# Performance work log

Measured on AMD Instinct MI355X. Metric: run time of the kernel, lower is better.

The kernel has to match this reference:

```python
import jax, jax.numpy as jnp
import numpy as np

N, D, IN, HID, OUT = 50000, 16, 128, 128, 64

def setup_inputs() -> dict:
    key = jax.random.key(0)
    ks = jax.random.split(key, 16)
    s = 0.05
    return {
        'feats':   jax.random.normal(ks[0], (N, IN), jnp.float32),
        'nbr':     jax.random.randint(ks[1], (N, D), 0, N, jnp.int32),
        'w_ih1':   jax.random.normal(ks[2], (4*IN, IN), jnp.float32)*s,
        'w_hh1':   jax.random.normal(ks[3], (4*IN, IN), jnp.float32)*s,
        'b_ih1':   jax.random.normal(ks[4], (4*IN,), jnp.float32)*s,
        'b_hh1':   jax.random.normal(ks[5], (4*IN,), jnp.float32)*s,
        'w_self1': jax.random.normal(ks[6], (HID, IN), jnp.float32)*s,
        'w_neigh1':jax.random.normal(ks[7], (HID, IN), jnp.float32)*s,
        'b1':      jax.random.normal(ks[8], (HID,), jnp.float32)*s,
        'w_ih2':   jax.random.normal(ks[9], (4*HID, HID), jnp.float32)*s,
        'w_hh2':   jax.random.normal(ks[10], (4*HID, HID), jnp.float32)*s,
        'b_ih2':   jax.random.normal(ks[11], (4*HID,), jnp.float32)*s,
        'b_hh2':   jax.random.normal(ks[12], (4*HID,), jnp.float32)*s,
        'w_self2': jax.random.normal(ks[13], (OUT, HID), jnp.float32)*s,
        'w_neigh2':jax.random.normal(ks[14], (OUT, HID), jnp.float32)*s,
        'b2':      jax.random.normal(ks[15], (OUT,), jnp.float32)*s,
    }

def _lstm_agg(m, w_ih, w_hh, b_ih, b_hh):
    # m: [N, D, F] gathered neighbor features; LSTM hidden size == F (DGL lstm reducer).
    n, d, f = m.shape
    b = b_ih + b_hh
    def step(carry, x_t):
        h, c = carry
        gates = x_t @ w_ih.T + h @ w_hh.T + b  # [N, 4F]
        i, fg, g, o = jnp.split(gates, 4, axis=-1)  # PyTorch gate order i,f,g,o
        i = jax.nn.sigmoid(i); fg = jax.nn.sigmoid(fg)
        g = jnp.tanh(g); o = jax.nn.sigmoid(o)
        c = fg * c + i * g
        h = o * jnp.tanh(c)
        return (h, c), None
    z = jnp.zeros((n, f), m.dtype)
    (h, _), _ = jax.lax.scan(step, (z, z), jnp.swapaxes(m, 0, 1))  # scan over degree axis
    return h  # [N, F] final hidden state

def _sage_conv(x, nbr, w_ih, w_hh, b_ih, b_hh, w_self, w_neigh, bias):
    m = x[nbr]  # [N, D, F] gather neighbor features
    h_neigh = _lstm_agg(m, w_ih, w_hh, b_ih, b_hh)
    return x @ w_self.T + h_neigh @ w_neigh.T + bias

def reference(feats, nbr, w_ih1, w_hh1, b_ih1, b_hh1, w_self1, w_neigh1, b1,
              w_ih2, w_hh2, b_ih2, b_hh2, w_self2, w_neigh2, b2):
    h = _sage_conv(feats, nbr, w_ih1, w_hh1, b_ih1, b_hh1, w_self1, w_neigh1, b1)
    h = jax.nn.relu(h)
    h = _sage_conv(h, nbr, w_ih2, w_hh2, b_ih2, b_hh2, w_self2, w_neigh2, b2)
    return jax.nn.sigmoid(h)
```

## Files before the change

### kernel.cpp

```cpp
#include <hip/hip_runtime.h>
#include <cstdint>
#include <cstddef>


constexpr int IN  = 128;
constexpr int DEG = 16;
#define LOG2E       1.4426950408889634f
#define TWO_LOG2E   2.8853900817779268f
#define NEG2_LOG2E -2.8853900817779268f

typedef short bf16x8 __attribute__((ext_vector_type(8)));
typedef float f32x4  __attribute__((ext_vector_type(4)));
typedef float f32x16 __attribute__((ext_vector_type(16)));
typedef unsigned int u32x4 __attribute__((ext_vector_type(4)));
typedef unsigned int u32x2 __attribute__((ext_vector_type(2)));

__device__ __forceinline__ float fsigmoid(float x) {
    float e = __expf(-x);
    return __builtin_amdgcn_rcpf(1.0f + e);
}
__device__ __forceinline__ uint32_t pack2bf16(float a, float b) {
    uint32_t ua = __float_as_uint(a) + 0x8000u;
    uint32_t ub = __float_as_uint(b) + 0x8000u;
    return (ua >> 16) | (ub & 0xFFFF0000u);
}


__global__ void k_pack_all(const float* __restrict__ w0, u32x4* __restrict__ f0,
                           const float* __restrict__ w1, u32x4* __restrict__ f1,
                           const float* __restrict__ w2, u32x4* __restrict__ f2,
                           const float* __restrict__ w3, u32x4* __restrict__ f3) {
    int gt = blockIdx.x * 256 + threadIdx.x;
    int which = gt >> 13;
    int tid  = gt & 8191;
    const float* wsrc = (which == 0) ? w0 : (which == 1) ? w1 : (which == 2) ? w2 : w3;
    u32x4* frag = (which == 0) ? f0 : (which == 1) ? f1 : (which == 2) ? f2 : f3;
    int lane = tid & 63;
    float v[8];
    int row;
    if ((which & 1) == 0) {
        int tile = (tid >> 6) & 15;
        int kst  = tid >> 10;
        row = tile * 32 + (lane & 31);
        int kbase = kst * 16 + (lane >> 5) * 8;
#pragma unroll
        for (int j = 0; j < 8; ++j) v[j] = wsrc[row * 128 + kbase + j];
    } else {
        int f  = tid >> 6;
        int ks = f & 3;
        int w8 = (f >> 2) & 7;
        int g  = f >> 5;
        row = g * 128 + w8 * 16 + (lane & 15);
        int kbase = ks * 32 + (lane >> 4) * 8;
#pragma unroll
        for (int j = 0; j < 8; ++j) v[j] = wsrc[row * 128 + kbase + j];
    }
    const float sc = ((row >> 7) == 2) ? TWO_LOG2E : LOG2E;
#pragma unroll
    for (int j = 0; j < 8; ++j) v[j] *= sc;
    u32x4 d;
    d.x = pack2bf16(v[0], v[1]);
    d.y = pack2bf16(v[2], v[3]);
    d.z = pack2bf16(v[4], v[5]);
    d.w = pack2bf16(v[6], v[7]);
    frag[tid] = d;
}

__global__ void k_pack_out(const float* __restrict__ ws1, const float* __restrict__ wn1,
                           u32x4* __restrict__ f1,
                           const float* __restrict__ ws2, const float* __restrict__ wn2,
                           u32x4* __restrict__ f2) {
    int t = blockIdx.x * 256 + threadIdx.x;
    int lane = t & 63;
    int row  = lane & 15;
    int kb   = (lane >> 4) * 8;
    float v[8];
    const float* ws; const float* wn; u32x4* dst; int p;
    if (t < 4096) { ws = ws1; wn = wn1; dst = f1; p = t; }
    else          { ws = ws2; wn = wn2; dst = f2; p = t - 4096; }
    int ks  = (p >> 6) & 7;
    int och = (p >> 9) * 16 + row;
    int kbase = ks * 32 + kb;
#pragma unroll
    for (int j = 0; j < 8; ++j) {
        int k = kbase + j;
        v[j] = (k < 128) ? ws[och * 128 + k] : wn[och * 128 + k - 128];
    }
    u32x4 d;
    d.x = pack2bf16(v[0], v[1]);
    d.y = pack2bf16(v[2], v[3]);
    d.z = pack2bf16(v[4], v[5]);
    d.w = pack2bf16(v[6], v[7]);
    dst[p] = d;
}

template <int CVT>
__global__ __launch_bounds__(256, 2) void k_xu(
    const void*   __restrict__ xin,
    ushort*       __restrict__ xbf,
    const u32x4*  __restrict__ wih,
    const float*  __restrict__ b_ih,
    const float*  __restrict__ b_hh,
    u32x2*        __restrict__ xu,
    int N)
{
    __shared__ u32x4 a_buf[16][66];

    const int tid   = threadIdx.x;
    const int lane  = tid & 63;
    const int w     = tid >> 6;
    const int mrow  = lane & 31;
    const int khalf = lane >> 5;
    const int node0 = blockIdx.x * 64;

    u32x4 wreg[8][4];
#pragma unroll
    for (int kst = 0; kst < 8; ++kst)
#pragma unroll
        for (int g = 0; g < 4; ++g)
            wreg[kst][g] = wih[(kst * 16 + g * 4 + w) * 64 + lane];

    float binit[4];
#pragma unroll
    for (int g = 0; g < 4; ++g) {
        int jj = g * 128 + w * 32 + mrow;
        binit[g] = (b_ih[jj] + b_hh[jj]) * ((g == 2) ? TWO_LOG2E : LOG2E);
    }

    {
        int m_st = tid >> 2, c4 = tid & 3;
        int gn = node0 + m_st; if (gn >= N) gn = N - 1;
        if constexpr (CVT) {
            const float* src = (const float*)xin + (size_t)gn * IN;
#pragma unroll
            for (int q = 0; q < 4; ++q) {
                int kg = q * 4 + c4;
                float4 f0 = *(const float4*)(src + kg * 8);
                float4 f1 = *(const float4*)(src + kg * 8 + 4);
                u32x4 d;
                d.x = pack2bf16(f0.x, f0.y);
                d.y = pack2bf16(f0.z, f0.w);
                d.z = pack2bf16(f1.x, f1.y);
                d.w = pack2bf16(f1.z, f1.w);
                a_buf[kg][m_st] = d;
                *(u32x4*)(xbf + (size_t)gn * IN + kg * 8) = d;
            }
        } else {
            const u32x4* src = (const u32x4*)((const ushort*)xin + (size_t)gn * IN);
#pragma unroll
            for (int q = 0; q < 4; ++q) {
                int kg = q * 4 + c4;
                a_buf[kg][m_st] = src[kg];
            }
        }
    }
    __syncthreads();

    const int coff = w * 32 + mrow;
#pragma unroll 1
    for (int Mt = 0; Mt < 2; ++Mt) {
        f32x16 acc[4];
#pragma unroll
        for (int g = 0; g < 4; ++g)
#pragma unroll
            for (int r = 0; r < 16; ++r) acc[g][r] = binit[g];

#pragma unroll
        for (int kst = 0; kst < 8; ++kst) {
            bf16x8 a = __builtin_bit_cast(bf16x8, a_buf[kst * 2 + khalf][Mt * 32 + mrow]);
#pragma unroll
            for (int g = 0; g < 4; ++g)
                acc[g] = __builtin_amdgcn_mfma_f32_32x32x16_bf16(
                    a, __builtin_bit_cast(bf16x8, wreg[kst][g]), acc[g], 0, 0, 0);
        }

#pragma unroll
        for (int r = 0; r < 16; ++r) {
            int m = Mt * 32 + (r & 3) + 8 * (r >> 2) + 4 * khalf;
            u32x2 d;
            d.x = pack2bf16(acc[0][r], acc[1][r]);
            d.y = pack2bf16(acc[2][r], acc[3][r]);
            xu[(size_t)(node0 + m) * 128 + coff] = d;
        }
    }
}

template <int NOUT, int ACT, typename OutT>
__global__ __launch_bounds__(512, 4) void k_lstm_fused(
    const u32x2*  __restrict__ xu,
    const int*    __restrict__ nbr,
    const u32x4*  __restrict__ whh,
    const u32x4*  __restrict__ wout,
    const float*  __restrict__ bout,
    const ushort* __restrict__ x_in,
    OutT*         __restrict__ out,
    int N)
{
    constexpr int HSTR = 272;
    __shared__ alignas(16) char h_lds[2][16 * HSTR];
    __shared__ uint32_t idxs[DEG * 16];

    const int tid  = threadIdx.x;
    const int lane = tid & 63;
    const int w    = tid >> 6;
    const int col  = lane & 15;
    const int l4   = lane >> 4;
    const int node0 = blockIdx.x * 16;

    if (tid < DEG * 16) {
        int m = tid & 15, t = tid >> 4;
        int gn = node0 + m; if (gn >= N) gn = N - 1;
        idxs[t * 16 + m] = (uint32_t)nbr[gn * DEG + t] << 10;
    }
    if (tid < 16 * HSTR / 16)
        ((u32x4*)h_lds[0])[tid] = u32x4{0u, 0u, 0u, 0u};

    u32x4 wreg[4][4];
#pragma unroll
    for (int g = 0; g < 4; ++g)
#pragma unroll
        for (int ks = 0; ks < 4; ++ks)
            wreg[g][ks] = whh[((g * 8 + w) * 4 + ks) * 64 + lane];

    float cst[4];
#pragma unroll
    for (int r = 0; r < 4; ++r) cst[r] = 0.0f;

    const char* xu_c = (const char*)xu;
    const uint32_t goff = (uint32_t)(w * 128 + l4 * 32);
    const int rd0 = col * HSTR + l4 * 16;
    const int wr0 = col * HSTR + w * 32 + l4 * 8;

    __syncthreads();

    u32x4 vv[2];
    {
        const char* p0 = xu_c + idxs[col] + goff;
        vv[0] = *(const u32x4*)(p0);
        vv[1] = *(const u32x4*)(p0 + 16);
    }

#pragma unroll 1
    for (int t = 0; t < DEG; ++t) {
        const char* hr = h_lds[t & 1];
        char*       hw = h_lds[(t + 1) & 1];

        f32x4 acc[4];
#pragma unroll
        for (int q = 0; q < 4; ++q) {
            uint32_t px = vv[q >> 1][(q & 1) * 2];
            uint32_t py = vv[q >> 1][(q & 1) * 2 + 1];
            acc[0][q] = __uint_as_float(px << 16);
            acc[1][q] = __uint_as_float(px & 0xFFFF0000u);
            acc[2][q] = __uint_as_float(py << 16);
            acc[3][q] = __uint_as_float(py & 0xFFFF0000u);
        }

        if (t + 1 < DEG) {
            const char* p0 = xu_c + idxs[(t + 1) * 16 + col] + goff;
            vv[0] = *(const u32x4*)(p0);
            vv[1] = *(const u32x4*)(p0 + 16);
        }

#pragma unroll
        for (int ks = 0; ks < 4; ++ks) {
            bf16x8 b = *(const bf16x8*)(hr + rd0 + ks * 64);
#pragma unroll
            for (int g = 0; g < 4; ++g)
                acc[g] = __builtin_amdgcn_mfma_f32_16x16x32_bf16(
                    __builtin_bit_cast(bf16x8, wreg[g][ks]), b, acc[g], 0, 0, 0);
        }

        float hv[4];
#pragma unroll
        for (int q = 0; q < 4; ++q) {
            float Ei = __builtin_amdgcn_exp2f(-acc[0][q]);
            float Eg = __builtin_amdgcn_exp2f(-acc[2][q]);
            float Ef = __builtin_amdgcn_exp2f(-acc[1][q]);
            float p  = (1.0f + Ei) * (1.0f + Eg);
            float num = __fmaf_rn(cst[q], p, (1.0f - Eg) * (1.0f + Ef));
            float cv = num * __builtin_amdgcn_rcpf(p * (1.0f + Ef));
            cst[q] = cv;
            float Eo = __builtin_amdgcn_exp2f(-acc[3][q]);
            float Ec = __builtin_amdgcn_exp2f(cv * NEG2_LOG2E);
            hv[q] = (1.0f - Ec) *
                    __builtin_amdgcn_rcpf((1.0f + Eo) * (1.0f + Ec));
        }
        u32x2 hp;
        hp.x = pack2bf16(hv[0], hv[1]);
        hp.y = pack2bf16(hv[2], hv[3]);
        *(u32x2*)(hw + wr0) = hp;

        __syncthreads();
    }

    if (NOUT == 128 || w < 4) {
        const char* hf = h_lds[0];
        const int otile = (NOUT == 128) ? w : (w & 3);
        const int och0  = otile * 16 + l4 * 4;
        const float4 bq = *(const float4*)(bout + och0);
        const int gn = node0 + col;
        const int gx = (gn < N) ? gn : (N - 1);
        f32x4 acc = {bq.x, bq.y, bq.z, bq.w};
#pragma unroll
        for (int ks = 0; ks < 8; ++ks) {
            u32x4 af = wout[(otile * 8 + ks) * 64 + lane];
            bf16x8 bf_;
            if (ks < 4)
                bf_ = *(const bf16x8*)((const char*)x_in + (size_t)gx * 256 +
                                       ks * 64 + l4 * 16);
            else
                bf_ = *(const bf16x8*)(hf + col * HSTR + (ks - 4) * 64 + l4 * 16);
            acc = __builtin_amdgcn_mfma_f32_16x16x32_bf16(
                __builtin_bit_cast(bf16x8, af), bf_, acc, 0, 0, 0);
        }
        if (gn < N) {
            float av[4];
#pragma unroll
            for (int q = 0; q < 4; ++q)
                av[q] = (ACT == 0) ? fmaxf(acc[q], 0.0f) : fsigmoid(acc[q]);
            if constexpr (sizeof(OutT) == 2) {
                u32x2 o;
                o.x = pack2bf16(av[0], av[1]);
                o.y = pack2bf16(av[2], av[3]);
                *(u32x2*)((ushort*)out + (size_t)gn * NOUT + och0) = o;
            } else {
                f32x4 o = {av[0], av[1], av[2], av[3]};
                *(f32x4*)((float*)out + (size_t)gn * NOUT + och0) = o;
            }
        }
    }
}

extern "C" void kernel_launch(void* const* d_in, const int* in_sizes, int n_in,
                              void* d_out, int out_size, void* d_ws, size_t ws_size,
                              hipStream_t stream)
{
    const float* feats    = (const float*)d_in[0];
    const int*   nbr      = (const int*)  d_in[1];
    const float* w_ih1    = (const float*)d_in[2];
    const float* w_hh1    = (const float*)d_in[3];
    const float* b_ih1    = (const float*)d_in[4];
    const float* b_hh1    = (const float*)d_in[5];
    const float* w_self1  = (const float*)d_in[6];
    const float* w_neigh1 = (const float*)d_in[7];
    const float* b1       = (const float*)d_in[8];
    const float* w_ih2    = (const float*)d_in[9];
    const float* w_hh2    = (const float*)d_in[10];
    const float* b_ih2    = (const float*)d_in[11];
    const float* b_hh2    = (const float*)d_in[12];
    const float* w_self2  = (const float*)d_in[13];
    const float* w_neigh2 = (const float*)d_in[14];
    const float* b2       = (const float*)d_in[15];
    float* out = (float*)d_out;

    const int N = in_sizes[0] / IN;
    const long long Nceil = (N + 63) & ~63LL;

    char* ws = (char*)d_ws;
    size_t off = 0;
    auto alloc = [&](size_t bytes) -> void* {
        void* p = (void*)(ws + off);
        off += (bytes + 255) & ~(size_t)255;
        return p;
    };
    u32x4*  wfrag_ih1 = (u32x4*)alloc(8192 * 16);
    u32x4*  wfrag_hh1 = (u32x4*)alloc(8192 * 16);
    u32x4*  wfrag_ih2 = (u32x4*)alloc(8192 * 16);
    u32x4*  wfrag_hh2 = (u32x4*)alloc(8192 * 16);
    u32x4*  wofrag1   = (u32x4*)alloc(4096 * 16);
    u32x4*  wofrag2   = (u32x4*)alloc(2048 * 16);
    ushort* feats_bf  = (ushort*)alloc((size_t)N * 128 * 2);
    ushort* out1      = (ushort*)alloc((size_t)N * 128 * 2);
    u32x2*  xu_buf    = (u32x2*)alloc((size_t)Nceil * 128 * 8);

    k_pack_all<<<dim3(128), dim3(256), 0, stream>>>(w_ih1, wfrag_ih1, w_hh1, wfrag_hh1,
                                                    w_ih2, wfrag_ih2, w_hh2, wfrag_hh2);
    k_pack_out<<<dim3(24), dim3(256), 0, stream>>>(w_self1, w_neigh1, wofrag1,
                                                   w_self2, w_neigh2, wofrag2);

    const int nblk64 = (int)(Nceil / 64);
    const int nblk16 = (N + 15) / 16;

    k_xu<1><<<dim3(nblk64), dim3(256), 0, stream>>>(feats, feats_bf, wfrag_ih1, b_ih1, b_hh1, xu_buf, N);
    k_lstm_fused<128, 0, ushort><<<dim3(nblk16), dim3(512), 0, stream>>>(
        xu_buf, nbr, wfrag_hh1, wofrag1, b1, feats_bf, out1, N);

    k_xu<0><<<dim3(nblk64), dim3(256), 0, stream>>>(out1, nullptr, wfrag_ih2, b_ih2, b_hh2, xu_buf, N);
    k_lstm_fused<64, 1, float><<<dim3(nblk16), dim3(512), 0, stream>>>(
        xu_buf, nbr, wfrag_hh2, wofrag2, b2, out1, out, N);
}
```

Baseline: 473.5 us.

## Make LSTM fused kernels persistent with atomic tile scheduling

Both fused LSTM kernels now launch a fixed grid of 512 blocks. Each block repeatedly claims 16-node tiles through a global atomic counter, which `k_pack_all` zeroes. This amortizes loading the recurrent weight fragments into registers across many tiles and removes block launch overhead. In exchange it adds an atomic plus an extra barrier per tile and caps residency at about two blocks per CU, which may reduce latency hiding in the barrier-heavy recurrence.

```diff
diff --git a/kernel.cpp b/kernel.cpp
--- a/kernel.cpp
+++ b/kernel.cpp
@@ -29,8 +29,10 @@
 __global__ void k_pack_all(const float* __restrict__ w0, u32x4* __restrict__ f0,
                            const float* __restrict__ w1, u32x4* __restrict__ f1,
                            const float* __restrict__ w2, u32x4* __restrict__ f2,
-                           const float* __restrict__ w3, u32x4* __restrict__ f3) {
+                           const float* __restrict__ w3, u32x4* __restrict__ f3,
+                           uint32_t* __restrict__ counters) {
     int gt = blockIdx.x * 256 + threadIdx.x;
+    if (gt < 2) counters[gt] = 0u;
     int which = gt >> 13;
     int tid  = gt & 8191;
     const float* wsrc = (which == 0) ? w0 : (which == 1) ? w1 : (which == 2) ? w2 : w3;
@@ -194,26 +196,19 @@
     const float*  __restrict__ bout,
     const ushort* __restrict__ x_in,
     OutT*         __restrict__ out,
-    int N)
+    uint32_t*     __restrict__ counter,
+    int ntiles, int N)
 {
     constexpr int HSTR = 272;
     __shared__ alignas(16) char h_lds[2][16 * HSTR];
     __shared__ uint32_t idxs[DEG * 16];
+    __shared__ int tile_s;
 
     const int tid  = threadIdx.x;
     const int lane = tid & 63;
     const int w    = tid >> 6;
     const int col  = lane & 15;
     const int l4   = lane >> 4;
-    const int node0 = blockIdx.x * 16;
-
-    if (tid < DEG * 16) {
-        int m = tid & 15, t = tid >> 4;
-        int gn = node0 + m; if (gn >= N) gn = N - 1;
-        idxs[t * 16 + m] = (uint32_t)nbr[gn * DEG + t] << 10;
-    }
-    if (tid < 16 * HSTR / 16)
-        ((u32x4*)h_lds[0])[tid] = u32x4{0u, 0u, 0u, 0u};
 
     u32x4 wreg[4][4];
 #pragma unroll
@@ -221,112 +216,128 @@
 #pragma unroll
         for (int ks = 0; ks < 4; ++ks)
             wreg[g][ks] = whh[((g * 8 + w) * 4 + ks) * 64 + lane];
-
-    float cst[4];
-#pragma unroll
-    for (int r = 0; r < 4; ++r) cst[r] = 0.0f;
 
     const char* xu_c = (const char*)xu;
     const uint32_t goff = (uint32_t)(w * 128 + l4 * 32);
     const int rd0 = col * HSTR + l4 * 16;
     const int wr0 = col * HSTR + w * 32 + l4 * 8;
 
-    __syncthreads();
-
-    u32x4 vv[2];
-    {
-        const char* p0 = xu_c + idxs[col] + goff;
-        vv[0] = *(const u32x4*)(p0);
-        vv[1] = *(const u32x4*)(p0 + 16);
-    }
-
-#pragma unroll 1
-    for (int t = 0; t < DEG; ++t) {
-        const char* hr = h_lds[t & 1];
-        char*       hw = h_lds[(t + 1) & 1];
-
-        f32x4 acc[4];
-#pragma unroll
-        for (int q = 0; q < 4; ++q) {
-            uint32_t px = vv[q >> 1][(q & 1) * 2];
-            uint32_t py = vv[q >> 1][(q & 1) * 2 + 1];
-            acc[0][q] = __uint_as_float(px << 16);
-            acc[1][q] = __uint_as_float(px & 0xFFFF0000u);
-            acc[2][q] = __uint_as_float(py << 16);
-            acc[3][q] = __uint_as_float(py & 0xFFFF0000u);
-        }
-
-        if (t + 1 < DEG) {
-            const char* p0 = xu_c + idxs[(t + 1) * 16 + col] + goff;
+    for (;;) {
+        if (tid == 0) tile_s = (int)atomicAdd(counter, 1u);
+        __syncthreads();
+        const int tile = tile_s;
+        if (tile >= ntiles) break;
+        const int node0 = tile * 16;
+
+        if (tid < DEG * 16) {
+            int m = tid & 15, t = tid >> 4;
+            int gn = node0 + m; if (gn >= N) gn = N - 1;
+            idxs[t * 16 + m] = (uint32_t)nbr[gn * DEG + t] << 10;
+        }
+        if (tid < 16 * HSTR / 16)
+            ((u32x4*)h_lds[0])[tid] = u32x4{0u, 0u, 0u, 0u};
+
+        float cst[4];
+#pragma unroll
+        for (int r = 0; r < 4; ++r) cst[r] = 0.0f;
+
+        __syncthreads();
+
+        u32x4 vv[2];
+        {
+            const char* p0 = xu_c + idxs[col] + goff;
             vv[0] = *(const u32x4*)(p0);
             vv[1] = *(const u32x4*)(p0 + 16);
         }
 
-#pragma unroll
-        for (int ks = 0; ks < 4; ++ks) {
-            bf16x8 b = *(const bf16x8*)(hr + rd0 + ks * 64);
-#pragma unroll
-            for (int g = 0; g < 4; ++g)
-                acc[g] = __builtin_amdgcn_mfma_f32_16x16x32_bf16(
-                    __builtin_bit_cast(bf16x8, wreg[g][ks]), b, acc[g], 0, 0, 0);
-        }
-
-        float hv[4];
-#pragma unroll
-        for (int q = 0; q < 4; ++q) {
-            float Ei = __builtin_amdgcn_exp2f(-acc[0][q]);
-            float Eg = __builtin_amdgcn_exp2f(-acc[2][q]);
-            float Ef = __builtin_amdgcn_exp2f(-acc[1][q]);
-            float p  = (1.0f + Ei) * (1.0f + Eg);
-            float num = __fmaf_rn(cst[q], p, (1.0f - Eg) * (1.0f + Ef));
-            float cv = num * __builtin_amdgcn_rcpf(p * (1.0f + Ef));
-            cst[q] = cv;
-            float Eo = __builtin_amdgcn_exp2f(-acc[3][q]);
-            float Ec = __builtin_amdgcn_exp2f(cv * NEG2_LOG2E);
-            hv[q] = (1.0f - Ec) *
-                    __builtin_amdgcn_rcpf((1.0f + Eo) * (1.0f + Ec));
-        }
-        u32x2 hp;
-        hp.x = pack2bf16(hv[0], hv[1]);
-        hp.y = pack2bf16(hv[2], hv[3]);
-        *(u32x2*)(hw + wr0) = hp;
-
-        __syncthreads();
-    }
-
-    if (NOUT == 128 || w < 4) {
-        const char* hf = h_lds[0];
-        const int otile = (NOUT == 128) ? w : (w & 3);
-        const int och0  = otile * 16 + l4 * 4;
-        const float4 bq = *(const float4*)(bout + och0);
-        const int gn = node0 + col;
-        const int gx = (gn < N) ? gn : (N - 1);
-        f32x4 acc = {bq.x, bq.y, bq.z, bq.w};
-#pragma unroll
-        for (int ks = 0; ks < 8; ++ks) {
-            u32x4 af = wout[(otile * 8 + ks) * 64 + lane];
-            bf16x8 bf_;
-            if (ks < 4)
-                bf_ = *(const bf16x8*)((const char*)x_in + (size_t)gx * 256 +
-                                       ks * 64 + l4 * 16);
-            else
-                bf_ = *(const bf16x8*)(hf + col * HSTR + (ks - 4) * 64 + l4 * 16);
-            acc = __builtin_amdgcn_mfma_f32_16x16x32_bf16(
-                __builtin_bit_cast(bf16x8, af), bf_, acc, 0, 0, 0);
-        }
-        if (gn < N) {
-            float av[4];
-#pragma unroll
-            for (int q = 0; q < 4; ++q)
-                av[q] = (ACT == 0) ? fmaxf(acc[q], 0.0f) : fsigmoid(acc[q]);
-            if constexpr (sizeof(OutT) == 2) {
-                u32x2 o;
-                o.x = pack2bf16(av[0], av[1]);
-                o.y = pack2bf16(av[2], av[3]);
-                *(u32x2*)((ushort*)out + (size_t)gn * NOUT + och0) = o;
-            } else {
-                f32x4 o = {av[0], av[1], av[2], av[3]};
-                *(f32x4*)((float*)out + (size_t)gn * NOUT + och0) = o;
+#pragma unroll 1
+        for (int t = 0; t < DEG; ++t) {
+            const char* hr = h_lds[t & 1];
+            char*       hw = h_lds[(t + 1) & 1];
+
+            f32x4 acc[4];
+#pragma unroll
+            for (int q = 0; q < 4; ++q) {
+                uint32_t px = vv[q >> 1][(q & 1) * 2];
+                uint32_t py = vv[q >> 1][(q & 1) * 2 + 1];
+                acc[0][q] = __uint_as_float(px << 16);
+                acc[1][q] = __uint_as_float(px & 0xFFFF0000u);
+                acc[2][q] = __uint_as_float(py << 16);
+                acc[3][q] = __uint_as_float(py & 0xFFFF0000u);
+            }
+
+            if (t + 1 < DEG) {
+                const char* p0 = xu_c + idxs[(t + 1) * 16 + col] + goff;
+                vv[0] = *(const u32x4*)(p0);
+                vv[1] = *(const u32x4*)(p0 + 16);
+            }
+
+#pragma unroll
+            for (int ks = 0; ks < 4; ++ks) {
+                bf16x8 b = *(const bf16x8*)(hr + rd0 + ks * 64);
+#pragma unroll
+                for (int g = 0; g < 4; ++g)
+                    acc[g] = __builtin_amdgcn_mfma_f32_16x16x32_bf16(
+                        __builtin_bit_cast(bf16x8, wreg[g][ks]), b, acc[g], 0, 0, 0);
+            }
+
+            float hv[4];
+#pragma unroll
+            for (int q = 0; q < 4; ++q) {
+                float Ei = __builtin_amdgcn_exp2f(-acc[0][q]);
+                float Eg = __builtin_amdgcn_exp2f(-acc[2][q]);
+                float Ef = __builtin_amdgcn_exp2f(-acc[1][q]);
+                float p  = (1.0f + Ei) * (1.0f + Eg);
+                float num = __fmaf_rn(cst[q], p, (1.0f - Eg) * (1.0f + Ef));
+                float cv = num * __builtin_amdgcn_rcpf(p * (1.0f + Ef));
+                cst[q] = cv;
+                float Eo = __builtin_amdgcn_exp2f(-acc[3][q]);
+                float Ec = __builtin_amdgcn_exp2f(cv * NEG2_LOG2E);
+                hv[q] = (1.0f - Ec) *
+                        __builtin_amdgcn_rcpf((1.0f + Eo) * (1.0f + Ec));
+            }
+            u32x2 hp;
+            hp.x = pack2bf16(hv[0], hv[1]);
+            hp.y = pack2bf16(hv[2], hv[3]);
+            *(u32x2*)(hw + wr0) = hp;
+
+            __syncthreads();
+        }
+
+        if (NOUT == 128 || w < 4) {
+            const char* hf = h_lds[0];
+            const int otile = (NOUT == 128) ? w : (w & 3);
+            const int och0  = otile * 16 + l4 * 4;
+            const float4 bq = *(const float4*)(bout + och0);
+            const int gn = node0 + col;
+            const int gx = (gn < N) ? gn : (N - 1);
+            f32x4 acc = {bq.x, bq.y, bq.z, bq.w};
+#pragma unroll
+            for (int ks = 0; ks < 8; ++ks) {
+                u32x4 af = wout[(otile * 8 + ks) * 64 + lane];
+                bf16x8 bf_;
+                if (ks < 4)
+                    bf_ = *(const bf16x8*)((const char*)x_in + (size_t)gx * 256 +
+                                           ks * 64 + l4 * 16);
+                else
+                    bf_ = *(const bf16x8*)(hf + col * HSTR + (ks - 4) * 64 + l4 * 16);
+                acc = __builtin_amdgcn_mfma_f32_16x16x32_bf16(
+                    __builtin_bit_cast(bf16x8, af), bf_, acc, 0, 0, 0);
+            }
+            if (gn < N) {
+                float av[4];
+#pragma unroll
+                for (int q = 0; q < 4; ++q)
+                    av[q] = (ACT == 0) ? fmaxf(acc[q], 0.0f) : fsigmoid(acc[q]);
+                if constexpr (sizeof(OutT) == 2) {
+                    u32x2 o;
+                    o.x = pack2bf16(av[0], av[1]);
+                    o.y = pack2bf16(av[2], av[3]);
+                    *(u32x2*)((ushort*)out + (size_t)gn * NOUT + och0) = o;
+                } else {
+                    f32x4 o = {av[0], av[1], av[2], av[3]};
+                    *(f32x4*)((float*)out + (size_t)gn * NOUT + och0) = o;
+                }
             }
         }
     }
@@ -370,23 +381,26 @@
     u32x4*  wfrag_hh2 = (u32x4*)alloc(8192 * 16);
     u32x4*  wofrag1   = (u32x4*)alloc(4096 * 16);
     u32x4*  wofrag2   = (u32x4*)alloc(2048 * 16);
+    uint32_t* counters = (uint32_t*)alloc(256);
     ushort* feats_bf  = (ushort*)alloc((size_t)N * 128 * 2);
     ushort* out1      = (ushort*)alloc((size_t)N * 128 * 2);
     u32x2*  xu_buf    = (u32x2*)alloc((size_t)Nceil * 128 * 8);
 
     k_pack_all<<<dim3(128), dim3(256), 0, stream>>>(w_ih1, wfrag_ih1, w_hh1, wfrag_hh1,
-                                                    w_ih2, wfrag_ih2, w_hh2, wfrag_hh2);
+                                                    w_ih2, wfrag_ih2, w_hh2, wfrag_hh2,
+                                                    counters);
     k_pack_out<<<dim3(24), dim3(256), 0, stream>>>(w_self1, w_neigh1, wofrag1,
                                                    w_self2, w_neigh2, wofrag2);
 
     const int nblk64 = (int)(Nceil / 64);
-    const int nblk16 = (N + 15) / 16;
+    const int ntiles = (N + 15) / 16;
+    const int PERSIST = 512;
 
     k_xu<1><<<dim3(nblk64), dim3(256), 0, stream>>>(feats, feats_bf, wfrag_ih1, b_ih1, b_hh1, xu_buf, N);
-    k_lstm_fused<128, 0, ushort><<<dim3(nblk16), dim3(512), 0, stream>>>(
-        xu_buf, nbr, wfrag_hh1, wofrag1, b1, feats_bf, out1, N);
+    k_lstm_fused<128, 0, ushort><<<dim3(PERSIST), dim3(512), 0, stream>>>(
+        xu_buf, nbr, wfrag_hh1, wofrag1, b1, feats_bf, out1, counters + 0, ntiles, N);
 
     k_xu<0><<<dim3(nblk64), dim3(256), 0, stream>>>(out1, nullptr, wfrag_ih2, b_ih2, b_hh2, xu_buf, N);
-    k_lstm_fused<64, 1, float><<<dim3(nblk16), dim3(512), 0, stream>>>(
-        xu_buf, nbr, wfrag_hh2, wofrag2, b2, out1, out, N);
-}
+    k_lstm_fused<64, 1, float><<<dim3(PERSIST), dim3(512), 0, stream>>>(
+        xu_buf, nbr, wfrag_hh2, wofrag2, b2, out1, out, counters + 1, ntiles, N);
+}
```

After: 490.7 us. 1.04x slower.
